# Kernel tuning notes

Measured on AMD Instinct MI355X. Metric: run time of the kernel, lower is better.

## Reference

```python
import jax, jax.numpy as jnp
import numpy as np

C_S, C_Z, C_H = 384, 128, 32
EPS = 1e-5


def setup_inputs() -> dict:
    key = jax.random.key(0)
    ks = jax.random.split(key, 8)
    N, L = 1, 512
    s = jax.random.normal(ks[0], (N, L, C_S), dtype=jnp.float32)
    ln_gamma = jnp.ones((C_S,), jnp.float32)
    ln_beta = jnp.zeros((C_S,), jnp.float32)
    sc = 1.0 / np.sqrt(C_S)
    w1 = jax.random.normal(ks[1], (C_S, C_H), jnp.float32) * sc
    b1 = jax.random.normal(ks[2], (C_H,), jnp.float32) * 0.02
    w2 = jax.random.normal(ks[3], (C_S, C_H), jnp.float32) * sc
    b2 = jax.random.normal(ks[4], (C_H,), jnp.float32) * 0.02
    w_out = jax.random.normal(ks[5], (C_H * C_H, C_Z), jnp.float32) * (1.0 / C_H)
    b_out = jax.random.normal(ks[6], (C_Z,), jnp.float32) * 0.02
    return {"s": s, "ln_gamma": ln_gamma, "ln_beta": ln_beta,
            "w1": w1, "b1": b1, "w2": w2, "b2": b2,
            "w_out": w_out, "b_out": b_out}


def reference(s, ln_gamma, ln_beta, w1, b1, w2, b2, w_out, b_out):
    # LayerNorm over c_s
    mu = jnp.mean(s, axis=-1, keepdims=True)
    var = jnp.mean(jnp.square(s - mu), axis=-1, keepdims=True)
    sn = (s - mu) * jax.lax.rsqrt(var + EPS) * ln_gamma + ln_beta
    # two projections: [N, L, c_hidden]
    a = jnp.einsum('nlc,ch->nlh', sn, w1) + b1
    b = jnp.einsum('nlc,ch->nlh', sn, w2) + b2
    # outer product + linear_out fused: (a_i ⊗ b_j) contracted with W_out
    w3 = w_out.reshape(C_H, C_H, C_Z)  # [h_a, h_b, c_z]
    z = jnp.einsum('nia,njb,abz->nijz', a, b, w3) + b_out
    return z  # [N, L, L, c_z]
```

## Files before the change

### kernel.cpp

```cpp
#include <hip/hip_runtime.h>

#define CS 384
#define CH 32
#define CZ 128
#define LL 512
#define C4 (CZ * CH)
#define EPSV 1e-5f

typedef __attribute__((ext_vector_type(8))) short bf16x8;
typedef __attribute__((ext_vector_type(4))) float f32x4;

static __device__ __forceinline__ unsigned short f2bf(float x) {
  union { float f; unsigned int u; } c; c.f = x;
  unsigned int r = c.u + 0x7FFFu + ((c.u >> 16) & 1u);
  return (unsigned short)(r >> 16);
}
static __device__ __forceinline__ unsigned int pk2(float lo, float hi) {
  return (unsigned int)f2bf(lo) | ((unsigned int)f2bf(hi) << 16);
}

__global__ __launch_bounds__(256) void prep_kernel(
    const float* __restrict__ s, const float* __restrict__ gamma,
    const float* __restrict__ beta,
    const float* __restrict__ w1, const float* __restrict__ b1,
    const float* __restrict__ w2, const float* __restrict__ b2,
    const float* __restrict__ w_out,
    unsigned short* __restrict__ Abf, unsigned short* __restrict__ Bbf,
    unsigned short* __restrict__ Wt) {
  __shared__ union {
    struct { float sn[CS]; float red[256]; float wred[8]; } ln;
    float wl[CH * CZ];
  } sm;
  int tid = threadIdx.x;

  if (blockIdx.x < LL) {
    int l = blockIdx.x;
    const float* srow = s + l * CS;
    float lsum = 0.f, lsq = 0.f;
    for (int c = tid; c < CS; c += 256) {
      float x = srow[c]; sm.ln.sn[c] = x; lsum += x; lsq += x * x;
    }
    #pragma unroll
    for (int off = 32; off > 0; off >>= 1) {
      lsum += __shfl_down(lsum, off);
      lsq  += __shfl_down(lsq, off);
    }
    int wv = tid >> 6;
    if ((tid & 63) == 0) { sm.ln.wred[wv] = lsum; sm.ln.wred[4 + wv] = lsq; }
    __syncthreads();
    float s1 = sm.ln.wred[0] + sm.ln.wred[1] + sm.ln.wred[2] + sm.ln.wred[3];
    float s2 = sm.ln.wred[4] + sm.ln.wred[5] + sm.ln.wred[6] + sm.ln.wred[7];
    float mu = s1 * (1.0f / CS);
    float var = s2 * (1.0f / CS) - mu * mu;
    float rstd = rsqrtf(var + EPSV);

    for (int c = tid; c < CS; c += 256)
      sm.ln.sn[c] = (sm.ln.sn[c] - mu) * rstd * gamma[c] + beta[c];
    __syncthreads();

    int o = tid & 63, q = tid >> 6;
    int h = o & 31;
    const float* w = (o < CH) ? w1 : w2;
    float acc = 0.f;
    int c0 = q * 96;
    #pragma unroll 8
    for (int c = c0; c < c0 + 96; ++c) acc += sm.ln.sn[c] * w[c * CH + h];
    sm.ln.red[tid] = acc; __syncthreads();
    if (tid < 64) {
      float r = sm.ln.red[tid] + sm.ln.red[tid + 64] + sm.ln.red[tid + 128] +
                sm.ln.red[tid + 192];
      if (o < CH) Abf[l * CH + h] = f2bf(r + b1[h]);
      else        Bbf[l * CH + h] = f2bf(r + b2[h]);
    }
  } else {
    int a = blockIdx.x - LL;
    const float4* Wg = (const float4*)(w_out + (size_t)a * CH * CZ);
    float4* Wl4 = (float4*)sm.wl;
    #pragma unroll
    for (int v = 0; v < 4; ++v) Wl4[tid + v * 256] = Wg[tid + v * 256];
    __syncthreads();
    int z = tid >> 1, bh = tid & 1;
    unsigned int dw[8];
    #pragma unroll
    for (int k = 0; k < 8; ++k) {
      unsigned short lo = f2bf(sm.wl[(bh * 16 + 2 * k) * CZ + z]);
      unsigned short hi = f2bf(sm.wl[(bh * 16 + 2 * k + 1) * CZ + z]);
      dw[k] = (unsigned int)lo | ((unsigned int)hi << 16);
    }
    unsigned int* dst =
        (unsigned int*)((char*)Wt + ((size_t)z * CH + a) * 64 + bh * 32);
    *(uint4*)dst = make_uint4(dw[0], dw[1], dw[2], dw[3]);
    *(uint4*)(dst + 4) = make_uint4(dw[4], dw[5], dw[6], dw[7]);
  }
}

__global__ __launch_bounds__(64) void tmat_kernel(
    const unsigned short* __restrict__ Bbf, const unsigned short* __restrict__ Wt,
    unsigned short* __restrict__ Tt) {
  int jt = blockIdx.x;
  int cq = blockIdx.y;
  int l = threadIdx.x;
  int q = l >> 4, r = l & 15;
  bf16x8 bfrag = *(const bf16x8*)(Bbf + (size_t)(jt * 16 + r) * CH + 8 * q);
  int j = jt * 16 + r;
  f32x4 zer = {0.f, 0.f, 0.f, 0.f};
  #pragma unroll
  for (int t = 0; t < 8; ++t) {
    int cbase = cq * 128 + t * 16;
    bf16x8 wfrag = *(const bf16x8*)(Wt + (size_t)(cbase + r) * CH + 8 * q);
    f32x4 acc = __builtin_amdgcn_mfma_f32_16x16x32_bf16(wfrag, bfrag, zer, 0, 0, 0);
    uint2 st;
    st.x = pk2(acc[0], acc[1]);
    st.y = pk2(acc[2], acc[3]);
    *(uint2*)(&Tt[(size_t)j * C4 + cbase + 4 * q]) = st;
  }
}

__global__ __launch_bounds__(512) void outer_mfma(
    const unsigned short* __restrict__ Abf, const unsigned short* __restrict__ Tt,
    const float* __restrict__ b_out, float* __restrict__ out) {
  unsigned n = blockIdx.x;
  int jt = n & 7;
  int it = n >> 3;
  int tid = threadIdx.x;
  int w = tid >> 6, l = tid & 63, q = l >> 4, r = l & 15;
  int ib = it * 16;

  bf16x8 af = *(const bf16x8*)(Abf + (size_t)(ib + r) * CH + 8 * q);

  f32x4 bo[8];
  #pragma unroll
  for (int zt = 0; zt < 8; ++zt) bo[zt] = *(const f32x4*)(b_out + zt * 16 + 4 * q);

  int j0 = jt * 64 + w * 8;
  float* orow = out + ((size_t)(ib + r) * LL) * CZ;

  #pragma unroll 2
  for (int jj = 0; jj < 8; ++jj) {
    int j = j0 + jj;
    const unsigned short* Tj = Tt + (size_t)j * C4;
    float* oj = orow + (size_t)j * CZ;
    #pragma unroll
    for (int zt = 0; zt < 8; ++zt) {
      bf16x8 tf = *(const bf16x8*)(Tj + (size_t)(zt * 16 + r) * CH + 8 * q);
      f32x4 d = __builtin_amdgcn_mfma_f32_16x16x32_bf16(tf, af, bo[zt], 0, 0, 0);
      *(f32x4*)(oj + zt * 16 + 4 * q) = d;
    }
  }
}

extern "C" void kernel_launch(void* const* d_in, const int* in_sizes, int n_in,
                              void* d_out, int out_size, void* d_ws, size_t ws_size,
                              hipStream_t stream) {
  const float* s     = (const float*)d_in[0];
  const float* gam   = (const float*)d_in[1];
  const float* bet   = (const float*)d_in[2];
  const float* w1    = (const float*)d_in[3];
  const float* b1    = (const float*)d_in[4];
  const float* w2    = (const float*)d_in[5];
  const float* b2    = (const float*)d_in[6];
  const float* w_out = (const float*)d_in[7];
  const float* b_out = (const float*)d_in[8];
  float* out = (float*)d_out;

  char* ws = (char*)d_ws;
  unsigned short* Abf = (unsigned short*)(ws);
  unsigned short* Bbf = (unsigned short*)(ws + 32768);
  unsigned short* Wt  = (unsigned short*)(ws + 65536);
  unsigned short* Tt  = (unsigned short*)(ws + 327680);

  prep_kernel<<<LL + CH, 256, 0, stream>>>(s, gam, bet, w1, b1, w2, b2, w_out,
                                           Abf, Bbf, Wt);
  tmat_kernel<<<dim3(32, 32), 64, 0, stream>>>(Bbf, Wt, Tt);
  outer_mfma<<<256, 512, 0, stream>>>(Abf, Tt, b_out, out);
}
```

Measured before the change: 42.31 us.

## Merge three kernels into one cooperative kernel with grid-wide syncs

Replaces the prep, T-matrix and outer-product launches with a single cooperative kernel of 256 blocks of 512 threads, separating the phases with grid.sync(). Each block now layer-norms two rows, and the first 32 blocks also convert the w_out weights. The T-matrix phase preloads all eight weight fragments before its MFMAs. This removes two kernel launch gaps, but costs two grid-wide barriers and leaves most blocks idle during the w_out conversion.

```diff
diff --git a/kernel.cpp b/kernel.cpp
--- a/kernel.cpp
+++ b/kernel.cpp
@@ -1,4 +1,7 @@
 #include <hip/hip_runtime.h>
+#include <hip/hip_cooperative_groups.h>
+
+namespace cg = cooperative_groups;
 
 #define CS 384
 #define CH 32
@@ -19,132 +22,147 @@
   return (unsigned int)f2bf(lo) | ((unsigned int)f2bf(hi) << 16);
 }
 
-__global__ __launch_bounds__(256) void prep_kernel(
+__global__ __launch_bounds__(512) void mega_kernel(
     const float* __restrict__ s, const float* __restrict__ gamma,
     const float* __restrict__ beta,
     const float* __restrict__ w1, const float* __restrict__ b1,
     const float* __restrict__ w2, const float* __restrict__ b2,
-    const float* __restrict__ w_out,
+    const float* __restrict__ w_out, const float* __restrict__ b_out,
     unsigned short* __restrict__ Abf, unsigned short* __restrict__ Bbf,
-    unsigned short* __restrict__ Wt) {
+    unsigned short* __restrict__ Wt, unsigned short* __restrict__ Tt,
+    float* __restrict__ out) {
+  cg::grid_group grid = cg::this_grid();
+  int n = blockIdx.x;
+  int tid = threadIdx.x;
   __shared__ union {
-    struct { float sn[CS]; float red[256]; float wred[8]; } ln;
+    struct { float sn[2][CS]; float red[2][256]; float wred[2][8]; } ln;
     float wl[CH * CZ];
   } sm;
-  int tid = threadIdx.x;
 
-  if (blockIdx.x < LL) {
-    int l = blockIdx.x;
-    const float* srow = s + l * CS;
+  {
+    int g = tid >> 8;
+    int t = tid & 255;
+    int l = 2 * n + g;
+    const float* srow = s + (size_t)l * CS;
     float lsum = 0.f, lsq = 0.f;
-    for (int c = tid; c < CS; c += 256) {
-      float x = srow[c]; sm.ln.sn[c] = x; lsum += x; lsq += x * x;
+    for (int c = t; c < CS; c += 256) {
+      float x = srow[c]; sm.ln.sn[g][c] = x; lsum += x; lsq += x * x;
     }
     #pragma unroll
     for (int off = 32; off > 0; off >>= 1) {
       lsum += __shfl_down(lsum, off);
       lsq  += __shfl_down(lsq, off);
     }
-    int wv = tid >> 6;
-    if ((tid & 63) == 0) { sm.ln.wred[wv] = lsum; sm.ln.wred[4 + wv] = lsq; }
+    int wv = t >> 6;
+    if ((t & 63) == 0) { sm.ln.wred[g][wv] = lsum; sm.ln.wred[g][4 + wv] = lsq; }
     __syncthreads();
-    float s1 = sm.ln.wred[0] + sm.ln.wred[1] + sm.ln.wred[2] + sm.ln.wred[3];
-    float s2 = sm.ln.wred[4] + sm.ln.wred[5] + sm.ln.wred[6] + sm.ln.wred[7];
+    float s1 = sm.ln.wred[g][0] + sm.ln.wred[g][1] + sm.ln.wred[g][2] + sm.ln.wred[g][3];
+    float s2 = sm.ln.wred[g][4] + sm.ln.wred[g][5] + sm.ln.wred[g][6] + sm.ln.wred[g][7];
     float mu = s1 * (1.0f / CS);
     float var = s2 * (1.0f / CS) - mu * mu;
     float rstd = rsqrtf(var + EPSV);
 
-    for (int c = tid; c < CS; c += 256)
-      sm.ln.sn[c] = (sm.ln.sn[c] - mu) * rstd * gamma[c] + beta[c];
+    for (int c = t; c < CS; c += 256)
+      sm.ln.sn[g][c] = (sm.ln.sn[g][c] - mu) * rstd * gamma[c] + beta[c];
     __syncthreads();
 
-    int o = tid & 63, q = tid >> 6;
+    int o = t & 63, qc = t >> 6;
     int h = o & 31;
     const float* w = (o < CH) ? w1 : w2;
     float acc = 0.f;
-    int c0 = q * 96;
+    int c0 = qc * 96;
     #pragma unroll 8
-    for (int c = c0; c < c0 + 96; ++c) acc += sm.ln.sn[c] * w[c * CH + h];
-    sm.ln.red[tid] = acc; __syncthreads();
-    if (tid < 64) {
-      float r = sm.ln.red[tid] + sm.ln.red[tid + 64] + sm.ln.red[tid + 128] +
-                sm.ln.red[tid + 192];
+    for (int c = c0; c < c0 + 96; ++c) acc += sm.ln.sn[g][c] * w[c * CH + h];
+    sm.ln.red[g][t] = acc; __syncthreads();
+    if (t < 64) {
+      float r = sm.ln.red[g][t] + sm.ln.red[g][t + 64] + sm.ln.red[g][t + 128] +
+                sm.ln.red[g][t + 192];
       if (o < CH) Abf[l * CH + h] = f2bf(r + b1[h]);
       else        Bbf[l * CH + h] = f2bf(r + b2[h]);
     }
-  } else {
-    int a = blockIdx.x - LL;
+  }
+  __syncthreads();
+
+  if (n < CH) {
+    int a = n;
     const float4* Wg = (const float4*)(w_out + (size_t)a * CH * CZ);
     float4* Wl4 = (float4*)sm.wl;
     #pragma unroll
-    for (int v = 0; v < 4; ++v) Wl4[tid + v * 256] = Wg[tid + v * 256];
+    for (int v = 0; v < 2; ++v) Wl4[tid + v * 512] = Wg[tid + v * 512];
     __syncthreads();
-    int z = tid >> 1, bh = tid & 1;
-    unsigned int dw[8];
+    if (tid < 256) {
+      int z = tid >> 1, bh = tid & 1;
+      unsigned int dw[8];
+      #pragma unroll
+      for (int k = 0; k < 8; ++k) {
+        unsigned short lo = f2bf(sm.wl[(bh * 16 + 2 * k) * CZ + z]);
+        unsigned short hi = f2bf(sm.wl[(bh * 16 + 2 * k + 1) * CZ + z]);
+        dw[k] = (unsigned int)lo | ((unsigned int)hi << 16);
+      }
+      unsigned int* dst =
+          (unsigned int*)((char*)Wt + ((size_t)z * CH + a) * 64 + bh * 32);
+      *(uint4*)dst = make_uint4(dw[0], dw[1], dw[2], dw[3]);
+      *(uint4*)(dst + 4) = make_uint4(dw[4], dw[5], dw[6], dw[7]);
+    }
+  }
+
+  grid.sync();
+
+  {
+    int wgid = n * 8 + (tid >> 6);
+    if (wgid < 1024) {
+      int jt = wgid >> 5;
+      int cq = wgid & 31;
+      int l = tid & 63;
+      int q = l >> 4, r = l & 15;
+      bf16x8 bfrag = *(const bf16x8*)(Bbf + (size_t)(jt * 16 + r) * CH + 8 * q);
+      int j = jt * 16 + r;
+      bf16x8 wfrag[8];
+      #pragma unroll
+      for (int t = 0; t < 8; ++t)
+        wfrag[t] = *(const bf16x8*)(Wt + (size_t)(cq * 128 + t * 16 + r) * CH + 8 * q);
+      f32x4 zer = {0.f, 0.f, 0.f, 0.f};
+      #pragma unroll
+      for (int t = 0; t < 8; ++t) {
+        int cbase = cq * 128 + t * 16;
+        f32x4 acc = __builtin_amdgcn_mfma_f32_16x16x32_bf16(wfrag[t], bfrag, zer, 0, 0, 0);
+        uint2 st;
+        st.x = pk2(acc[0], acc[1]);
+        st.y = pk2(acc[2], acc[3]);
+        *(uint2*)(&Tt[(size_t)j * C4 + cbase + 4 * q]) = st;
+      }
+    }
+  }
+
+  grid.sync();
+
+  {
+    int jt = n & 7;
+    int it = n >> 3;
+    int w = tid >> 6, l = tid & 63, q = l >> 4, r = l & 15;
+    int ib = it * 16;
+
+    bf16x8 af = *(const bf16x8*)(Abf + (size_t)(ib + r) * CH + 8 * q);
+
+    f32x4 bo[8];
     #pragma unroll
-    for (int k = 0; k < 8; ++k) {
-      unsigned short lo = f2bf(sm.wl[(bh * 16 + 2 * k) * CZ + z]);
-      unsigned short hi = f2bf(sm.wl[(bh * 16 + 2 * k + 1) * CZ + z]);
-      dw[k] = (unsigned int)lo | ((unsigned int)hi << 16);
-    }
-    unsigned int* dst =
-        (unsigned int*)((char*)Wt + ((size_t)z * CH + a) * 64 + bh * 32);
-    *(uint4*)dst = make_uint4(dw[0], dw[1], dw[2], dw[3]);
-    *(uint4*)(dst + 4) = make_uint4(dw[4], dw[5], dw[6], dw[7]);
-  }
-}
+    for (int zt = 0; zt < 8; ++zt)
+      bo[zt] = *(const f32x4*)(b_out + zt * 16 + 4 * q);
 
-__global__ __launch_bounds__(64) void tmat_kernel(
-    const unsigned short* __restrict__ Bbf, const unsigned short* __restrict__ Wt,
-    unsigned short* __restrict__ Tt) {
-  int jt = blockIdx.x;
-  int cq = blockIdx.y;
-  int l = threadIdx.x;
-  int q = l >> 4, r = l & 15;
-  bf16x8 bfrag = *(const bf16x8*)(Bbf + (size_t)(jt * 16 + r) * CH + 8 * q);
-  int j = jt * 16 + r;
-  f32x4 zer = {0.f, 0.f, 0.f, 0.f};
-  #pragma unroll
-  for (int t = 0; t < 8; ++t) {
-    int cbase = cq * 128 + t * 16;
-    bf16x8 wfrag = *(const bf16x8*)(Wt + (size_t)(cbase + r) * CH + 8 * q);
-    f32x4 acc = __builtin_amdgcn_mfma_f32_16x16x32_bf16(wfrag, bfrag, zer, 0, 0, 0);
-    uint2 st;
-    st.x = pk2(acc[0], acc[1]);
-    st.y = pk2(acc[2], acc[3]);
-    *(uint2*)(&Tt[(size_t)j * C4 + cbase + 4 * q]) = st;
-  }
-}
+    int j0 = jt * 64 + w * 8;
+    float* orow = out + ((size_t)ib + r) * LL * CZ;
 
-__global__ __launch_bounds__(512) void outer_mfma(
-    const unsigned short* __restrict__ Abf, const unsigned short* __restrict__ Tt,
-    const float* __restrict__ b_out, float* __restrict__ out) {
-  unsigned n = blockIdx.x;
-  int jt = n & 7;
-  int it = n >> 3;
-  int tid = threadIdx.x;
-  int w = tid >> 6, l = tid & 63, q = l >> 4, r = l & 15;
-  int ib = it * 16;
-
-  bf16x8 af = *(const bf16x8*)(Abf + (size_t)(ib + r) * CH + 8 * q);
-
-  f32x4 bo[8];
-  #pragma unroll
-  for (int zt = 0; zt < 8; ++zt) bo[zt] = *(const f32x4*)(b_out + zt * 16 + 4 * q);
-
-  int j0 = jt * 64 + w * 8;
-  float* orow = out + ((size_t)(ib + r) * LL) * CZ;
-
-  #pragma unroll 2
-  for (int jj = 0; jj < 8; ++jj) {
-    int j = j0 + jj;
-    const unsigned short* Tj = Tt + (size_t)j * C4;
-    float* oj = orow + (size_t)j * CZ;
-    #pragma unroll
-    for (int zt = 0; zt < 8; ++zt) {
-      bf16x8 tf = *(const bf16x8*)(Tj + (size_t)(zt * 16 + r) * CH + 8 * q);
-      f32x4 d = __builtin_amdgcn_mfma_f32_16x16x32_bf16(tf, af, bo[zt], 0, 0, 0);
-      *(f32x4*)(oj + zt * 16 + 4 * q) = d;
+    #pragma unroll 2
+    for (int jj = 0; jj < 8; ++jj) {
+      int j = j0 + jj;
+      const unsigned short* Tj = Tt + (size_t)j * C4;
+      float* oj = orow + (size_t)j * CZ;
+      #pragma unroll
+      for (int zt = 0; zt < 8; ++zt) {
+        bf16x8 tf = *(const bf16x8*)(Tj + (size_t)(zt * 16 + r) * CH + 8 * q);
+        f32x4 d = __builtin_amdgcn_mfma_f32_16x16x32_bf16(tf, af, bo[zt], 0, 0, 0);
+        *(f32x4*)(oj + zt * 16 + 4 * q) = d;
+      }
     }
   }
 }
@@ -169,8 +187,9 @@
   unsigned short* Wt  = (unsigned short*)(ws + 65536);
   unsigned short* Tt  = (unsigned short*)(ws + 327680);
 
-  prep_kernel<<<LL + CH, 256, 0, stream>>>(s, gam, bet, w1, b1, w2, b2, w_out,
-                                           Abf, Bbf, Wt);
-  tmat_kernel<<<dim3(32, 32), 64, 0, stream>>>(Bbf, Wt, Tt);
-  outer_mfma<<<256, 512, 0, stream>>>(Abf, Tt, b_out, out);
+  void* args[] = {(void*)&s, (void*)&gam, (void*)&bet, (void*)&w1, (void*)&b1,
+                  (void*)&w2, (void*)&b2, (void*)&w_out, (void*)&b_out,
+                  (void*)&Abf, (void*)&Bbf, (void*)&Wt, (void*)&Tt, (void*)&out};
+  hipLaunchCooperativeKernel((void*)mega_kernel, dim3(256), dim3(512), args, 0,
+                             stream);
 }
```

New measurement: 109.2 us. 2.58x slower.

## Warp-specialize outer kernel: MFMA warps stage tiles in LDS, store warps write coalesced rows

Applied to the files above, without the earlier changes.

The outer-product kernel is split into producer and consumer waves. Four waves compute MFMA tiles and write them into a double-buffered, XOR-swizzled LDS buffer. The other four waves read that buffer and write full contiguous 512-byte output rows, so global stores coalesce better than the earlier 16-byte scattered stores, and compute overlaps with the previous step's stores. The cost is half as many waves doing MFMA, 64KB of LDS per block, and a block-wide barrier on every step.

```diff
diff --git a/kernel.cpp b/kernel.cpp
--- a/kernel.cpp
+++ b/kernel.cpp
@@ -119,32 +119,53 @@
 __global__ __launch_bounds__(512) void outer_mfma(
     const unsigned short* __restrict__ Abf, const unsigned short* __restrict__ Tt,
     const float* __restrict__ b_out, float* __restrict__ out) {
+  __shared__ float buf[2][4][16 * CZ];
   unsigned n = blockIdx.x;
   int jt = n & 7;
   int it = n >> 3;
   int tid = threadIdx.x;
-  int w = tid >> 6, l = tid & 63, q = l >> 4, r = l & 15;
+  int w = tid >> 6, l = tid & 63;
   int ib = it * 16;
+  int j0 = jt * 64;
 
-  bf16x8 af = *(const bf16x8*)(Abf + (size_t)(ib + r) * CH + 8 * q);
+  if (w < 4) {
+    int q = l >> 4, r = l & 15;
+    bf16x8 af = *(const bf16x8*)(Abf + (size_t)(ib + r) * CH + 8 * q);
+    f32x4 bo[8];
+    #pragma unroll
+    for (int zt = 0; zt < 8; ++zt)
+      bo[zt] = *(const f32x4*)(b_out + zt * 16 + 4 * q);
 
-  f32x4 bo[8];
-  #pragma unroll
-  for (int zt = 0; zt < 8; ++zt) bo[zt] = *(const f32x4*)(b_out + zt * 16 + 4 * q);
-
-  int j0 = jt * 64 + w * 8;
-  float* orow = out + ((size_t)(ib + r) * LL) * CZ;
-
-  #pragma unroll 2
-  for (int jj = 0; jj < 8; ++jj) {
-    int j = j0 + jj;
-    const unsigned short* Tj = Tt + (size_t)j * C4;
-    float* oj = orow + (size_t)j * CZ;
-    #pragma unroll
-    for (int zt = 0; zt < 8; ++zt) {
-      bf16x8 tf = *(const bf16x8*)(Tj + (size_t)(zt * 16 + r) * CH + 8 * q);
-      f32x4 d = __builtin_amdgcn_mfma_f32_16x16x32_bf16(tf, af, bo[zt], 0, 0, 0);
-      *(f32x4*)(oj + zt * 16 + 4 * q) = d;
+    for (int t = 0; t <= 16; ++t) {
+      if (t < 16) {
+        int j = j0 + 4 * t + w;
+        const unsigned short* Tj = Tt + (size_t)j * C4;
+        float* myb = buf[t & 1][w];
+        #pragma unroll
+        for (int zt = 0; zt < 8; ++zt) {
+          bf16x8 tf = *(const bf16x8*)(Tj + (size_t)(zt * 16 + r) * CH + 8 * q);
+          f32x4 d = __builtin_amdgcn_mfma_f32_16x16x32_bf16(tf, af, bo[zt], 0, 0, 0);
+          int p = (4 * zt + q) ^ (r & 7);
+          *(f32x4*)(myb + r * CZ + p * 4) = d;
+        }
+      }
+      __syncthreads();
+    }
+  } else {
+    int c = w - 4;
+    int lam = l & 31, half = l >> 5;
+    for (int t = 0; t <= 16; ++t) {
+      if (t >= 1) {
+        int j = j0 + 4 * (t - 1) + c;
+        const float* myb = buf[(t - 1) & 1][c];
+        #pragma unroll
+        for (int ip = 0; ip < 8; ++ip) {
+          int row = 2 * ip + half;
+          f32x4 v = *(const f32x4*)(myb + row * CZ + ((lam ^ (row & 7)) * 4));
+          *(f32x4*)(out + ((size_t)(ib + row) * LL + j) * CZ + lam * 4) = v;
+        }
+      }
+      __syncthreads();
     }
   }
 }
```

After: 43.49 us. 2.8% more time.

## Keep T fragments in registers per wave and iterate over i tiles

Applied to the files above, without the earlier changes.

Each wave in outer_mfma now owns one j and a 128-row chunk of i. It loads the full T_j fragment set (8 bf16x8) into registers once and loops over 8 i-tiles, prefetching the next A fragment. Blocks are mapped so that consecutive block indices on the same XCD cover adjacent j. This removes the repeated T_j loads from the inner loop, at the cost of more registers and a different output write pattern.

```diff
diff --git a/kernel.cpp b/kernel.cpp
--- a/kernel.cpp
+++ b/kernel.cpp
@@ -120,32 +120,39 @@
     const unsigned short* __restrict__ Abf, const unsigned short* __restrict__ Tt,
     const float* __restrict__ b_out, float* __restrict__ out) {
   unsigned n = blockIdx.x;
-  int jt = n & 7;
-  int it = n >> 3;
   int tid = threadIdx.x;
   int w = tid >> 6, l = tid & 63, q = l >> 4, r = l & 15;
-  int ib = it * 16;
+  unsigned xcd = n & 7, idx = n >> 3;
+  unsigned wu = (xcd * 32 + idx) * 8 + w;
+  int j  = wu >> 2;
+  int ic = wu & 3;
 
-  bf16x8 af = *(const bf16x8*)(Abf + (size_t)(ib + r) * CH + 8 * q);
+  const unsigned short* Tj = Tt + (size_t)j * C4;
+  bf16x8 tf[8];
+  #pragma unroll
+  for (int zt = 0; zt < 8; ++zt)
+    tf[zt] = *(const bf16x8*)(Tj + (size_t)(zt * 16 + r) * CH + 8 * q);
 
   f32x4 bo[8];
   #pragma unroll
-  for (int zt = 0; zt < 8; ++zt) bo[zt] = *(const f32x4*)(b_out + zt * 16 + 4 * q);
+  for (int zt = 0; zt < 8; ++zt)
+    bo[zt] = *(const f32x4*)(b_out + zt * 16 + 4 * q);
 
-  int j0 = jt * 64 + w * 8;
-  float* orow = out + ((size_t)(ib + r) * LL) * CZ;
+  int ib0 = ic * 128;
+  bf16x8 af = *(const bf16x8*)(Abf + (size_t)(ib0 + r) * CH + 8 * q);
 
-  #pragma unroll 2
-  for (int jj = 0; jj < 8; ++jj) {
-    int j = j0 + jj;
-    const unsigned short* Tj = Tt + (size_t)j * C4;
-    float* oj = orow + (size_t)j * CZ;
+  for (int t = 0; t < 8; ++t) {
+    int ib = ib0 + t * 16;
+    int ibn = ib0 + ((t + 1) & 7) * 16;
+    bf16x8 afn = *(const bf16x8*)(Abf + (size_t)(ibn + r) * CH + 8 * q);
+
+    float* oj = out + ((size_t)(ib + r) * LL + j) * CZ + 4 * q;
     #pragma unroll
     for (int zt = 0; zt < 8; ++zt) {
-      bf16x8 tf = *(const bf16x8*)(Tj + (size_t)(zt * 16 + r) * CH + 8 * q);
-      f32x4 d = __builtin_amdgcn_mfma_f32_16x16x32_bf16(tf, af, bo[zt], 0, 0, 0);
-      *(f32x4*)(oj + zt * 16 + 4 * q) = d;
+      f32x4 d = __builtin_amdgcn_mfma_f32_16x16x32_bf16(tf[zt], af, bo[zt], 0, 0, 0);
+      *(f32x4*)(oj + zt * 16) = d;
     }
+    af = afn;
   }
 }
 
```

After: 40.80 us. -3.6%, faster.
